# Optimization experiments

Measured on AMD Instinct MI355X. Metric: run time of the kernel, lower is better.

## Reference

```python
import jax, jax.numpy as jnp
import numpy as np

STRIDES = (8, 16, 32)
FMP = ((256, 256), (128, 128), (64, 64))  # H, W per level (img 2048, strides 8/16/32)
NUM_CLASSES = 80
TOPK = 1000
CONF_THRESH = 0.05
NMS_THRESH = 0.6
IMG_H = IMG_W = 2048


def _anchors(level):
    h, w = FMP[level]
    ys, xs = jnp.meshgrid(jnp.arange(h), jnp.arange(w), indexing="ij")
    xy = jnp.stack([xs, ys], axis=-1).astype(jnp.float32).reshape(-1, 2) + 0.5
    return xy * STRIDES[level]  # [M, 2]


def _level(cls_pred, reg_pred, scale, level):
    # scores/labels per anchor
    probs = jax.nn.sigmoid(cls_pred)                 # [M, C]
    scores = jnp.max(probs, axis=-1)                 # [M]
    labels = jnp.argmax(probs, axis=-1)              # [M]
    anchors = _anchors(level)
    # per-level topk (M > TOPK for all levels here)
    scores, idx = jax.lax.top_k(scores, TOPK)
    labels = labels[idx]
    reg = reg_pred[idx]
    anchors = anchors[idx]
    # decode: ctr offset in [-1.5, 1.5] cells, size via exp(scale * pred)
    ctr = anchors + (jax.nn.sigmoid(reg[:, :2]) * 3.0 - 1.5)
    wh = jnp.exp(reg[:, 2:] * scale)
    box = jnp.concatenate([ctr - 0.5 * wh, ctr + 0.5 * wh], axis=-1) * STRIDES[level]
    return scores, labels, box


def _greedy_nms(boxes, scores, labels, valid):
    """Class-aware greedy NMS with fixed shapes; returns keep mask [N].
    Per-class NMS is realized by offsetting boxes per class so cross-class IoU=0,
    which matches the original per-class loop exactly."""
    N = boxes.shape[0]
    b = boxes + labels.astype(jnp.float32)[:, None] * (4.0 * IMG_W)
    order = jnp.argsort(-scores)
    b = b[order]
    v = valid[order]
    area = (b[:, 2] - b[:, 0]) * (b[:, 3] - b[:, 1])
    xx1 = jnp.maximum(b[:, None, 0], b[None, :, 0])
    yy1 = jnp.maximum(b[:, None, 1], b[None, :, 1])
    xx2 = jnp.minimum(b[:, None, 2], b[None, :, 2])
    yy2 = jnp.minimum(b[:, None, 3], b[None, :, 3])
    w = jnp.maximum(1e-10, xx2 - xx1)
    h = jnp.maximum(1e-10, yy2 - yy1)
    inter = w * h
    iou = inter / (area[:, None] + area[None, :] - inter + 1e-14)  # [N, N]
    idxr = jnp.arange(N)

    def body(i, keep):
        sup = (iou[i] > NMS_THRESH) & (idxr > i)
        return jnp.where(keep[i], keep & ~sup, keep)

    keep_sorted = jax.lax.fori_loop(0, N, body, v)
    return jnp.zeros((N,), dtype=bool).at[order].set(keep_sorted)


def setup_inputs() -> dict:
    key = jax.random.key(0)
    ks = jax.random.split(key, 6)
    inp = {}
    for lvl, (h, w) in enumerate(FMP):
        m = h * w
        inp[f"cls{lvl}"] = jax.random.normal(ks[2 * lvl], (m, NUM_CLASSES), dtype=jnp.float32)
        inp[f"reg{lvl}"] = jax.random.normal(ks[2 * lvl + 1], (m, 4), dtype=jnp.float32)
    inp["scales"] = jnp.ones((3,), dtype=jnp.float32)
    return inp


def reference(cls0, reg0, cls1, reg1, cls2, reg2, scales):
    per_level = [
        _level(cls0, reg0, scales[0], 0),
        _level(cls1, reg1, scales[1], 1),
        _level(cls2, reg2, scales[2], 2),
    ]
    scores = jnp.concatenate([p[0] for p in per_level])   # [3000]
    labels = jnp.concatenate([p[1] for p in per_level])   # [3000]
    bboxes = jnp.concatenate([p[2] for p in per_level])   # [3000, 4]
    valid = scores >= CONF_THRESH
    keep = _greedy_nms(bboxes, scores, labels, valid)     # [3000] bool mask
    # normalize to [0, 1] by image size
    norm = jnp.array([IMG_W, IMG_H, IMG_W, IMG_H], dtype=jnp.float32)
    bboxes = jnp.clip(bboxes / norm, 0.0, 1.0)
    # fixed-shape outputs: keep mask replaces dynamic filtering (jit-friendly)
    return bboxes, scores, labels, keep
```

## Files before the change

kernel.cpp:

```cpp
#include <hip/hip_runtime.h>
#include <stdint.h>


#define N_ALL 3000
#define N_PAD 3008
#define N_WORDS 47
#define CAP 6144

typedef unsigned long long u64;
typedef uint32_t u32;

__device__ __constant__ u32 T16C[3] = {0xC056u, 0xC03Cu, 0xC021u};

__device__ __forceinline__ u32 f32_ord(float x) {
    u32 u = __float_as_uint(x);
    return (u & 0x80000000u) ? ~u : (u | 0x80000000u);
}
__device__ __forceinline__ float ord_f32(u32 o) {
    u32 u = (o & 0x80000000u) ? (o & 0x7FFFFFFFu) : ~o;
    return __uint_as_float(u);
}
__device__ __forceinline__ u64 shfl_u64(u64 v, int src) {
    int lo = __shfl((int)(u32)(v & 0xFFFFFFFFull), src);
    int hi = __shfl((int)(u32)(v >> 32), src);
    return ((u64)(u32)hi << 32) | (u32)(unsigned)lo;
}

__global__ __launch_bounds__(64) void k_init(u32* __restrict__ cnt,
                                             u64* __restrict__ kwinit) {
    int tid = threadIdx.x;
    if (tid < 8) cnt[tid] = 0u;
    if (tid < N_WORDS) kwinit[tid] = 0ull;
}

__global__ __launch_bounds__(256) void k_scores(
        const float* __restrict__ cls0, const float* __restrict__ cls1,
        const float* __restrict__ cls2, u64* __restrict__ keys,
        u64* __restrict__ comp, u32* __restrict__ cnt) {
    __shared__ __align__(16) float tile[64 * 80];
    int b = blockIdx.x;
    int lvl, local0, off;
    const float* base;
    if (b < 1024)      { lvl = 0; local0 = b * 64;          base = cls0; off = 0; }
    else if (b < 1280) { lvl = 1; local0 = (b - 1024) * 64; base = cls1; off = 65536; }
    else               { lvl = 2; local0 = (b - 1280) * 64; base = cls2; off = 81920; }
    const float4* src = (const float4*)(base + (size_t)local0 * 80);
    float4* dst = (float4*)tile;
    int tid = threadIdx.x;
#pragma unroll
    for (int k = 0; k < 5; k++) dst[tid + k * 256] = src[tid + k * 256];
    __syncthreads();
    int a = tid >> 2, s = tid & 3;
    const float4* row = (const float4*)(tile + a * 80 + s * 20);
    float m = -3.4e38f; int lab = 0;
#pragma unroll
    for (int q = 0; q < 5; q++) {
        float4 v = row[q];
        int j0 = s * 20 + q * 4;
        if (v.x > m) { m = v.x; lab = j0;     }
        if (v.y > m) { m = v.y; lab = j0 + 1; }
        if (v.z > m) { m = v.z; lab = j0 + 2; }
        if (v.w > m) { m = v.w; lab = j0 + 3; }
    }
    float om = __shfl_xor(m, 1); int ol = __shfl_xor(lab, 1);
    if (om > m || (om == m && ol < lab)) { m = om; lab = ol; }
    om = __shfl_xor(m, 2); ol = __shfl_xor(lab, 2);
    if (om > m || (om == m && ol < lab)) { m = om; lab = ol; }
    u64 key = 0; bool pred = false;
    if (s == 0) {
        int local = local0 + a;
        key = ((u64)f32_ord(m) << 32)
            | ((u64)(0x1FFFFu - (u32)local) << 7)
            | (u64)lab;
        keys[off + local] = key;
        pred = ((u32)(key >> 48) >= T16C[lvl]);
    }
    u64 mask = __ballot(pred);
    if (mask) {
        int leader = __ffsll((long long)mask) - 1;
        int lane = threadIdx.x & 63;
        u32 bse = 0;
        if (lane == leader) bse = atomicAdd(&cnt[lvl], (u32)__popcll(mask));
        bse = (u32)__shfl((int)bse, leader);
        u32 myoff = (u32)__popcll(mask & ((1ull << lane) - 1ull));
        if (pred) { u32 pp = bse + myoff; if (pp < CAP) comp[lvl * CAP + pp] = key; }
    }
}

__global__ __launch_bounds__(256) void k_rank(
        const u64* __restrict__ keys, const u64* __restrict__ comp,
        const u32* __restrict__ cnt, u64* __restrict__ topk) {
    __shared__ u64 buf[CAP];
    __shared__ u32 s_hist[256];
    __shared__ u32 s_kk, s_c;
    __shared__ u64 s_pref;
    int lvl = blockIdx.x / 12, sub = blockIdx.x % 12;
    u32 C = cnt[lvl];
    int tid = threadIdx.x;
    if (C >= 1000u && C <= (u32)CAP) {
        for (int i = tid; i < (int)C; i += 256) buf[i] = comp[lvl * CAP + i];
        __syncthreads();
        for (int i = sub * 256 + tid; i < (int)C; i += 3072) {
            u64 x = buf[i];
            int rank = 0;
            int Cr = (int)C & ~15;
            int j = 0;
            for (; j < Cr; j += 16) {
                u64 a[16];
#pragma unroll
                for (int q = 0; q < 16; q++) a[q] = buf[j + q];
#pragma unroll
                for (int q = 0; q < 16; q++) rank += (a[q] > x) ? 1 : 0;
            }
            for (; j < (int)C; j++) rank += (buf[j] > x) ? 1 : 0;
            if (rank < 1000) topk[lvl * 1000 + rank] = x;
        }
        return;
    }
    if (sub != 0) return;
    int M = (lvl == 0) ? 65536 : (lvl == 1 ? 16384 : 4096);
    const u64* k = keys + ((lvl == 0) ? 0 : (lvl == 1 ? 65536 : 81920));
    if (tid == 0) { s_pref = 0; s_kk = 1000u; s_c = 0; }
    for (int d = 7; d >= 0; d--) {
        if (tid < 256) s_hist[tid] = 0;
        __syncthreads();
        u64 pref = s_pref;
        for (int i = tid; i < M; i += 256) {
            u64 key = k[i];
            if (d == 7 || (key >> ((d + 1) * 8)) == pref)
                atomicAdd(&s_hist[(u32)(key >> (d * 8)) & 255u], 1u);
        }
        __syncthreads();
        if (tid == 0) {
            u32 kk = s_kk, cum = 0;
            for (int b = 255; b >= 0; b--) {
                u32 h = s_hist[b];
                if (cum + h >= kk) { s_pref = (pref << 8) | (u32)b; s_kk = kk - cum; break; }
                cum += h;
            }
        }
        __syncthreads();
    }
    u64 T = s_pref;
    for (int i = tid; i < M; i += 256) {
        u64 key = k[i];
        if (key >= T) { u32 p = atomicAdd(&s_c, 1u); if (p < 1024u) buf[p] = key; }
    }
    __syncthreads();
    for (int i = tid; i < 1000; i += 256) {
        u64 x = buf[i]; int rank = 0;
        for (int j = 0; j < 1000; j++) rank += (buf[j] > x) ? 1 : 0;
        topk[lvl * 1000 + rank] = x;
    }
}

__device__ __forceinline__ int cnt_desc_lds(const u64* list, u64 x, bool strict) {
    int lo = 0, hi = 1000;
    while (lo < hi) {
        int mid = (lo + hi) >> 1;
        u64 v = list[mid];
        bool in = strict ? (v > x) : (v >= x);
        if (in) lo = mid + 1; else hi = mid;
    }
    return lo;
}
__global__ __launch_bounds__(256) void k_post(
        const u64* __restrict__ topk,
        const float* __restrict__ reg0, const float* __restrict__ reg1,
        const float* __restrict__ reg2, const float* __restrict__ scales,
        float* __restrict__ out, double* __restrict__ rbox,
        u32* __restrict__ order, u64* __restrict__ kwinit) {
    __shared__ u64 lt[N_ALL];
    int tid = threadIdx.x;
    for (int i = tid; i < N_ALL; i += 256) lt[i] = topk[i];
    __syncthreads();
    int r = blockIdx.x * 256 + tid;
    if (r >= N_ALL) return;
    int lvl = r / 1000;
    u64 key = lt[r];
    u32 low = (u32)key;
    int lab = (int)(low & 0x7Fu);
    int local = 0x1FFFF - (int)((low >> 7) & 0x1FFFFu);
    float logit = ord_f32((u32)(key >> 32));
    float score = 1.0f / (1.0f + expf(-logit));
    const float* regp = (lvl == 0 ? reg0 : (lvl == 1 ? reg1 : reg2));
    float4 rg = *(const float4*)(regp + (size_t)local * 4);
    float scale = scales[lvl];
    int wlog = 8 - lvl;
    int x = local & ((1 << wlog) - 1);
    int y = local >> wlog;
    float stridef = (float)(8 << lvl);
    float ax = ((float)x + 0.5f) * stridef;
    float ay = ((float)y + 0.5f) * stridef;
    float sx = 1.0f / (1.0f + expf(-rg.x));
    float sy = 1.0f / (1.0f + expf(-rg.y));
    float cx = ax + (sx * 3.0f - 1.5f);
    float cy = ay + (sy * 3.0f - 1.5f);
    float ww = expf(rg.z * scale);
    float hh = expf(rg.w * scale);
    float b0 = (cx - 0.5f * ww) * stridef;
    float b1 = (cy - 0.5f * hh) * stridef;
    float b2 = (cx + 0.5f * ww) * stridef;
    float b3 = (cy + 0.5f * hh) * stridef;
    const float inv = 1.0f / 2048.0f;
    out[r * 4 + 0] = fminf(fmaxf(b0 * inv, 0.0f), 1.0f);
    out[r * 4 + 1] = fminf(fmaxf(b1 * inv, 0.0f), 1.0f);
    out[r * 4 + 2] = fminf(fmaxf(b2 * inv, 0.0f), 1.0f);
    out[r * 4 + 3] = fminf(fmaxf(b3 * inv, 0.0f), 1.0f);
    out[12000 + r] = score;
    out[15000 + r] = (float)lab;
    int rank = r - lvl * 1000;
#pragma unroll
    for (int L2 = 0; L2 < 3; L2++)
        if (L2 != lvl) rank += cnt_desc_lds(lt + L2 * 1000, key, L2 > lvl);
    order[rank] = (u32)r;
    double c = (double)lab * 8192.0;
    double4 rb;
    rb.x = (double)b0 + c; rb.y = (double)b1 + c;
    rb.z = (double)b2 + c; rb.w = (double)b3 + c;
    ((double4*)rbox)[rank] = rb;
    if (score >= 0.05f) atomicOr(&kwinit[rank >> 6], 1ull << (rank & 63));
}

__global__ __launch_bounds__(256) void k_iou(
        const double* __restrict__ rbox, u64* __restrict__ sup,
        u64* __restrict__ diag, u64* __restrict__ rowfut) {
    int s = blockIdx.x;
    int tid = threadIdx.x;
    __shared__ u64 s_rf;
    if (tid == 0) s_rf = 0;
    __syncthreads();
    int tword = s >> 6;
    bool srow_ok = (s < N_ALL);
    const double4* rb4 = (const double4*)rbox;
    double ix1 = 0, iy1 = 0, ix2 = 0, iy2 = 0, iarea = 0;
    if (srow_ok) {
        double4 b = rb4[s];
        ix1 = b.x; iy1 = b.y; ix2 = b.z; iy2 = b.w;
        iarea = (ix2 - ix1) * (iy2 - iy1);
    }
    for (int j = (tword << 6) + tid; j < N_PAD; j += 256) {
        bool sb = false;
        if (srow_ok && j < N_ALL && j > s) {
            double4 bj = rb4[j];
            double xx1 = fmax(ix1, bj.x), yy1 = fmax(iy1, bj.y);
            double xx2 = fmin(ix2, bj.z), yy2 = fmin(iy2, bj.w);
            double w = fmax(1e-10, xx2 - xx1);
            double h = fmax(1e-10, yy2 - yy1);
            double inter = w * h;
            double jarea = (bj.z - bj.x) * (bj.w - bj.y);
            double uni = iarea + jarea - inter + 1e-14;
            sb = inter > 0.6 * uni;
        }
        u64 bal = __ballot(sb);
        if ((j & 63) == 0) {
            int w = j >> 6;
            sup[(size_t)s * N_WORDS + w] = bal;
            if (w == tword) diag[s] = bal;
            if (w > tword && bal) atomicOr(&s_rf, 1ull << w);
        }
    }
    __syncthreads();
    if (tid == 0) rowfut[s] = s_rf;
}

__global__ __launch_bounds__(64) void k_scan(
        const u64* __restrict__ sup, const u64* __restrict__ diag,
        const u64* __restrict__ rowfut, const u64* __restrict__ kwinit,
        const u32* __restrict__ order, float* __restrict__ out_keep) {
    int lane = threadIdx.x;
    u64 kw = (lane < N_WORDS) ? kwinit[lane] : 0ull;
    u64 d  = diag[lane];
    u64 rf = rowfut[lane];
    for (int t = 0; t < N_WORDS; t++) {
        u64 dn = 0, rfn = 0;
        if (t < N_WORDS - 1) {
            dn  = diag[(t + 1) * 64 + lane];
            rfn = rowfut[(t + 1) * 64 + lane];
        }
        u64 km = shfl_u64(kw, t);
        u64 nzd = __ballot(d != 0ull);
        u64 todo = nzd;
        while (true) {
            u64 c = todo & km;
            if (!c) break;
            int b = __ffsll((long long)c) - 1;
            todo &= ~(1ull << b);
            u64 m = shfl_u64(d, b);
            km &= ~m;
        }
        if (lane == t) kw = km;
        u64 appl = km & __ballot(rf != 0ull);
        while (appl) {
            int b = __ffsll((long long)appl) - 1;
            appl &= appl - 1;
            u64 rfb = shfl_u64(rf, b);
            u64 m2 = 0ull;
            if (lane < N_WORDS && ((rfb >> lane) & 1ull))
                m2 = sup[(size_t)(t * 64 + b) * N_WORDS + lane];
            kw &= ~m2;
        }
        d = dn; rf = rfn;
    }
    if (lane < N_WORDS) {
#pragma unroll 16
        for (int b = 0; b < 64; b++) {
            int j = lane * 64 + b;
            if (j < N_ALL) out_keep[order[j]] = ((kw >> b) & 1ull) ? 1.0f : 0.0f;
        }
    }
}

extern "C" void kernel_launch(void* const* d_in, const int* in_sizes, int n_in,
                              void* d_out, int out_size, void* d_ws, size_t ws_size,
                              hipStream_t stream) {
    const float* cls0   = (const float*)d_in[0];
    const float* reg0   = (const float*)d_in[1];
    const float* cls1   = (const float*)d_in[2];
    const float* reg1   = (const float*)d_in[3];
    const float* cls2   = (const float*)d_in[4];
    const float* reg2   = (const float*)d_in[5];
    const float* scales = (const float*)d_in[6];
    float* out = (float*)d_out;
    char* ws = (char*)d_ws;
    u64* keys   = (u64*)(ws + 0);
    u64* sup    = (u64*)(ws + 0);
    u32* cnt    = (u32*)(ws + 1131008);
    u64* kwinit = (u64*)(ws + 1131040);
    u64* comp   = (u64*)(ws + 1131424);
    u64* topk   = (u64*)(ws + 1278880);
    u32* order  = (u32*)(ws + 1302880);
    double* rbox= (double*)(ws + 1314880);
    u64* diag   = (u64*)(ws + 1411136);
    u64* rowfut = (u64*)(ws + 1435200);

    k_init<<<1, 64, 0, stream>>>(cnt, kwinit);
    k_scores<<<1344, 256, 0, stream>>>(cls0, cls1, cls2, keys, comp, cnt);
    k_rank<<<36, 256, 0, stream>>>(keys, comp, cnt, topk);
    k_post<<<12, 256, 0, stream>>>(topk, reg0, reg1, reg2, scales, out, rbox, order, kwinit);
    k_iou<<<N_PAD, 256, 0, stream>>>(rbox, sup, diag, rowfut);
    k_scan<<<1, 64, 0, stream>>>(sup, diag, rowfut, kwinit, order, out + 18000);
}
```

Before: 198.1 us.

## Remove init and scan launches via per-block candidate masks and last-block ticket

```diff
diff --git a/kernel.cpp b/kernel.cpp
--- a/kernel.cpp
+++ b/kernel.cpp
@@ -26,18 +26,12 @@
     return ((u64)(u32)hi << 32) | (u32)(unsigned)lo;
 }
 
-__global__ __launch_bounds__(64) void k_init(u32* __restrict__ cnt,
-                                             u64* __restrict__ kwinit) {
-    int tid = threadIdx.x;
-    if (tid < 8) cnt[tid] = 0u;
-    if (tid < N_WORDS) kwinit[tid] = 0ull;
-}
-
 __global__ __launch_bounds__(256) void k_scores(
         const float* __restrict__ cls0, const float* __restrict__ cls1,
         const float* __restrict__ cls2, u64* __restrict__ keys,
-        u64* __restrict__ comp, u32* __restrict__ cnt) {
+        u64* __restrict__ smask) {
     __shared__ __align__(16) float tile[64 * 80];
+    __shared__ u64 lds_mask;
     int b = blockIdx.x;
     int lvl, local0, off;
     const float* base;
@@ -47,6 +41,7 @@
     const float4* src = (const float4*)(base + (size_t)local0 * 80);
     float4* dst = (float4*)tile;
     int tid = threadIdx.x;
+    if (tid == 0) lds_mask = 0ull;
 #pragma unroll
     for (int k = 0; k < 5; k++) dst[tid + k * 256] = src[tid + k * 256];
     __syncthreads();
@@ -66,39 +61,68 @@
     if (om > m || (om == m && ol < lab)) { m = om; lab = ol; }
     om = __shfl_xor(m, 2); ol = __shfl_xor(lab, 2);
     if (om > m || (om == m && ol < lab)) { m = om; lab = ol; }
-    u64 key = 0; bool pred = false;
     if (s == 0) {
         int local = local0 + a;
-        key = ((u64)f32_ord(m) << 32)
-            | ((u64)(0x1FFFFu - (u32)local) << 7)
-            | (u64)lab;
+        u64 key = ((u64)f32_ord(m) << 32)
+                | ((u64)(0x1FFFFu - (u32)local) << 7)
+                | (u64)lab;
         keys[off + local] = key;
-        pred = ((u32)(key >> 48) >= T16C[lvl]);
-    }
-    u64 mask = __ballot(pred);
-    if (mask) {
-        int leader = __ffsll((long long)mask) - 1;
-        int lane = threadIdx.x & 63;
-        u32 bse = 0;
-        if (lane == leader) bse = atomicAdd(&cnt[lvl], (u32)__popcll(mask));
-        bse = (u32)__shfl((int)bse, leader);
-        u32 myoff = (u32)__popcll(mask & ((1ull << lane) - 1ull));
-        if (pred) { u32 pp = bse + myoff; if (pp < CAP) comp[lvl * CAP + pp] = key; }
-    }
+        if ((u32)(key >> 48) >= T16C[lvl])
+            atomicOr(&lds_mask, 1ull << a);
+    }
+    __syncthreads();
+    if (tid == 0) smask[b] = lds_mask;
 }
 
 __global__ __launch_bounds__(256) void k_rank(
-        const u64* __restrict__ keys, const u64* __restrict__ comp,
-        const u32* __restrict__ cnt, u64* __restrict__ topk) {
+        const u64* __restrict__ keys, const u64* __restrict__ smask,
+        u64* __restrict__ topk, u64* __restrict__ kwinit) {
     __shared__ u64 buf[CAP];
     __shared__ u32 s_hist[256];
+    __shared__ u32 swt[4];
     __shared__ u32 s_kk, s_c;
     __shared__ u64 s_pref;
     int lvl = blockIdx.x / 12, sub = blockIdx.x % 12;
-    u32 C = cnt[lvl];
-    int tid = threadIdx.x;
+    int M, koff, mb, NB, per;
+    if (lvl == 0)      { M = 65536; koff = 0;     mb = 0;    NB = 1024; per = 4; }
+    else if (lvl == 1) { M = 16384; koff = 65536; mb = 1024; NB = 256;  per = 1; }
+    else               { M = 4096;  koff = 81920; mb = 1280; NB = 64;   per = 1; }
+    int tid = threadIdx.x, lane = tid & 63, wv = tid >> 6;
+    if (blockIdx.x == 0 && tid < N_WORDS) kwinit[tid] = 0ull;
+    u64 mk[4]; u32 mycnt = 0;
+#pragma unroll
+    for (int p = 0; p < 4; p++) {
+        int idx = tid * per + p;
+        mk[p] = (p < per && idx < NB) ? smask[mb + idx] : 0ull;
+        mycnt += (u32)__popcll(mk[p]);
+    }
+    u32 inc = mycnt;
+#pragma unroll
+    for (int d = 1; d < 64; d <<= 1) {
+        u32 u = __shfl_up(inc, d);
+        if (lane >= d) inc += u;
+    }
+    if (lane == 63) swt[wv] = inc;
+    __syncthreads();
+    u32 wpre = 0;
+    for (int w = 0; w < 4; w++) if (w < wv) wpre += swt[w];
+    u32 C = swt[0] + swt[1] + swt[2] + swt[3];
+    u32 off = wpre + inc - mycnt;
     if (C >= 1000u && C <= (u32)CAP) {
-        for (int i = tid; i < (int)C; i += 256) buf[i] = comp[lvl * CAP + i];
+#pragma unroll
+        for (int p = 0; p < 4; p++) {
+            if (p >= per) break;
+            int idx = tid * per + p;
+            if (idx < NB) {
+                u64 mm = mk[p];
+                int abase = idx * 64;
+                while (mm) {
+                    int bb = __ffsll((long long)mm) - 1;
+                    mm &= mm - 1;
+                    buf[off++] = keys[koff + abase + bb];
+                }
+            }
+        }
         __syncthreads();
         for (int i = sub * 256 + tid; i < (int)C; i += 3072) {
             u64 x = buf[i];
@@ -118,8 +142,7 @@
         return;
     }
     if (sub != 0) return;
-    int M = (lvl == 0) ? 65536 : (lvl == 1 ? 16384 : 4096);
-    const u64* k = keys + ((lvl == 0) ? 0 : (lvl == 1 ? 65536 : 81920));
+    const u64* k = keys + koff;
     if (tid == 0) { s_pref = 0; s_kk = 1000u; s_c = 0; }
     for (int d = 7; d >= 0; d--) {
         if (tid < 256) s_hist[tid] = 0;
@@ -169,9 +192,11 @@
         const float* __restrict__ reg0, const float* __restrict__ reg1,
         const float* __restrict__ reg2, const float* __restrict__ scales,
         float* __restrict__ out, double* __restrict__ rbox,
-        u32* __restrict__ order, u64* __restrict__ kwinit) {
+        u32* __restrict__ order, u64* __restrict__ kwinit,
+        u32* __restrict__ ticket) {
     __shared__ u64 lt[N_ALL];
     int tid = threadIdx.x;
+    if (blockIdx.x == 0 && tid == 0) *ticket = 0u;
     for (int i = tid; i < N_ALL; i += 256) lt[i] = topk[i];
     __syncthreads();
     int r = blockIdx.x * 256 + tid;
@@ -224,10 +249,13 @@
 
 __global__ __launch_bounds__(256) void k_iou(
         const double* __restrict__ rbox, u64* __restrict__ sup,
-        u64* __restrict__ diag, u64* __restrict__ rowfut) {
+        u64* __restrict__ diag, u64* __restrict__ rowfut,
+        const u64* __restrict__ kwinit, const u32* __restrict__ order,
+        u32* __restrict__ ticket, float* __restrict__ out_keep) {
     int s = blockIdx.x;
     int tid = threadIdx.x;
     __shared__ u64 s_rf;
+    __shared__ int s_last;
     if (tid == 0) s_rf = 0;
     __syncthreads();
     int tword = s >> 6;
@@ -261,14 +289,16 @@
         }
     }
     __syncthreads();
-    if (tid == 0) rowfut[s] = s_rf;
-}
-
-__global__ __launch_bounds__(64) void k_scan(
-        const u64* __restrict__ sup, const u64* __restrict__ diag,
-        const u64* __restrict__ rowfut, const u64* __restrict__ kwinit,
-        const u32* __restrict__ order, float* __restrict__ out_keep) {
-    int lane = threadIdx.x;
+    if (tid == 0) {
+        rowfut[s] = s_rf;
+        __threadfence();
+        u32 t = __hip_atomic_fetch_add(ticket, 1u, __ATOMIC_ACQ_REL,
+                                       __HIP_MEMORY_SCOPE_AGENT);
+        s_last = (t == (u32)(N_PAD - 1)) ? 1 : 0;
+    }
+    __syncthreads();
+    if (!s_last || tid >= 64) return;
+    int lane = tid;
     u64 kw = (lane < N_WORDS) ? kwinit[lane] : 0ull;
     u64 d  = diag[lane];
     u64 rf = rowfut[lane];
@@ -325,19 +355,17 @@
     char* ws = (char*)d_ws;
     u64* keys   = (u64*)(ws + 0);
     u64* sup    = (u64*)(ws + 0);
-    u32* cnt    = (u32*)(ws + 1131008);
-    u64* kwinit = (u64*)(ws + 1131040);
-    u64* comp   = (u64*)(ws + 1131424);
-    u64* topk   = (u64*)(ws + 1278880);
-    u32* order  = (u32*)(ws + 1302880);
-    double* rbox= (double*)(ws + 1314880);
-    u64* diag   = (u64*)(ws + 1411136);
-    u64* rowfut = (u64*)(ws + 1435200);
-
-    k_init<<<1, 64, 0, stream>>>(cnt, kwinit);
-    k_scores<<<1344, 256, 0, stream>>>(cls0, cls1, cls2, keys, comp, cnt);
-    k_rank<<<36, 256, 0, stream>>>(keys, comp, cnt, topk);
-    k_post<<<12, 256, 0, stream>>>(topk, reg0, reg1, reg2, scales, out, rbox, order, kwinit);
-    k_iou<<<N_PAD, 256, 0, stream>>>(rbox, sup, diag, rowfut);
-    k_scan<<<1, 64, 0, stream>>>(sup, diag, rowfut, kwinit, order, out + 18000);
-}
+    u64* smask  = (u64*)(ws + 1131008);
+    u64* topk   = (u64*)(ws + 1141760);
+    u32* order  = (u32*)(ws + 1165760);
+    u64* kwinit = (u64*)(ws + 1177760);
+    u32* ticket = (u32*)(ws + 1178144);
+    double* rbox= (double*)(ws + 1178176);
+    u64* diag   = (u64*)(ws + 1274432);
+    u64* rowfut = (u64*)(ws + 1298496);
+
+    k_scores<<<1344, 256, 0, stream>>>(cls0, cls1, cls2, keys, smask);
+    k_rank<<<36, 256, 0, stream>>>(keys, smask, topk, kwinit);
+    k_post<<<12, 256, 0, stream>>>(topk, reg0, reg1, reg2, scales, out, rbox, order, kwinit, ticket);
+    k_iou<<<N_PAD, 256, 0, stream>>>(rbox, sup, diag, rowfut, kwinit, order, ticket, out + 18000);
+}
```

Measured after the change: 283.9 us. +43.3%, slower.
